# Performance work log

Measured on AMD Instinct MI355X. Metric: run time of the kernel, lower is better.

## Reference

```python
import jax, jax.numpy as jnp
import numpy as np

B, T, N, F_IN, F_OUT = 2, 8, 8192, 128, 32

def setup_inputs() -> dict:
    key = jax.random.key(0)
    k1, k2, k3, k4 = jax.random.split(key, 4)
    inp = jax.random.normal(k1, (B, T, N, F_IN), dtype=jnp.float32)
    adj = jax.random.randint(k2, (N, N), 0, 2, dtype=jnp.int32)
    # xavier_uniform with gain=1.414 ~ std = gain*sqrt(2/(fan_in+fan_out)); gaussian approx
    w_std = 1.414 * np.sqrt(2.0 / (F_IN + F_OUT))
    a_std = 1.414 * np.sqrt(2.0 / (2 * F_OUT + N))
    W = jax.random.normal(k3, (F_IN, F_OUT), dtype=jnp.float32) * w_std
    a = jax.random.normal(k4, (2 * F_OUT, N), dtype=jnp.float32) * a_std
    return {"inp": inp, "adj": adj, "W": W, "a": a}

def reference(inp, adj, W, a):
    # h: [B,T,N,out]
    h = jnp.einsum('btni,io->btno', inp, W)
    out = W.shape[1]
    # mask[j,i] = 1 if j is a neighbor of i (original: torch.where(adj[:, i] > 0))
    mask = (adj > 0).astype(h.dtype)
    # neighbor sum per destination node i: [B,T,N,out]
    nbr = jnp.einsum('ji,btjo->btio', mask, h)
    a1 = a[:out].T   # [N, out], per-node first half of attention vector
    a2 = a[out:].T   # [N, out], per-node second half
    # scalar score per (b,t,i); broadcast across j in the original attention matrix.
    # no-neighbor case coincides since nbr is zero there.
    s = jnp.einsum('btno,no->btn', h, a1) + jnp.einsum('btno,no->btn', nbr, a2)
    # h_prime[b,t,i,:] = s[b,t,i] * sum_j h[b,t,j,:]  (attention row is constant)
    h_prime = s[..., None] * jnp.sum(h, axis=2, keepdims=True)
    return jax.nn.relu(h_prime)
```

## Files before the change

### kernel.cpp

```cpp
#include <hip/hip_runtime.h>

#define BT 16
#define NN 8192
#define FIN 128
#define FOUT 32
#define NB 512
#define SPLITK 4
#define KSPAN (NN / SPLITK)
#define BKK 64
#define PADK 72

typedef __attribute__((ext_vector_type(8))) short short8;
typedef __attribute__((ext_vector_type(4))) float float4v;

__device__ __forceinline__ float bf2f(unsigned short u) {
    unsigned v = ((unsigned)u) << 16;
    float f;
    __builtin_memcpy(&f, &v, 4);
    return f;
}
__device__ __forceinline__ unsigned short f2bf(float f) {
    unsigned u;
    __builtin_memcpy(&u, &f, 4);
    u += 0x7FFFu + ((u >> 16) & 1u);
    return (unsigned short)(u >> 16);
}

__device__ __forceinline__ void load_lds16(const unsigned short* g, unsigned short* l) {
    __builtin_amdgcn_global_load_lds((const __attribute__((address_space(1))) void*)g,
                                     (__attribute__((address_space(3))) void*)l, 16, 0, 0);
}

__global__ void sniff_dtype(const unsigned* __restrict__ Wraw, unsigned* __restrict__ flag,
                            float* __restrict__ sumh) {
    int lane = threadIdx.x;
    unsigned u = Wraw[lane];
    float f = bf2f((unsigned short)(u & 0xFFFFu));
    float af = fabsf(f);
    bool plaus = (af > 1e-5f) && (af < 1e3f);
    unsigned long long msk = __ballot(plaus);
    if (lane == 0) flag[0] = (__popcll(msk) >= 32) ? 1u : 0u;
#pragma unroll
    for (int r = 0; r < 8; ++r) sumh[lane + 64 * r] = 0.f;
}

__launch_bounds__(256)
__global__ void k1(const void* __restrict__ inp_raw, const void* __restrict__ W_raw,
                   unsigned short* __restrict__ Ht, float* __restrict__ sumh,
                   float4* __restrict__ s2v, const unsigned* __restrict__ flagp) {
    __shared__ __align__(16) unsigned short Wt[32 * 136];
    int bid = blockIdx.x;
    const int tid = threadIdx.x;

    if (bid < 128) {
        float4 z; z.x = z.y = z.z = z.w = 0.f;
        s2v[bid * 256 + tid] = z;
        return;
    }
    bid -= 128;
    const int bt = bid >> 6;
    const int j0 = (bid & 63) * 128;
    const bool isbf = (*flagp != 0u);

    if (isbf) {
        const unsigned short* Wb = (const unsigned short*)W_raw;
#pragma unroll
        for (int r = 0; r < 16; ++r) {
            int idx = tid + 256 * r, i = idx >> 5, o = idx & 31;
            Wt[o * 136 + i] = Wb[idx];
        }
    } else {
        const float* Wf = (const float*)W_raw;
#pragma unroll
        for (int r = 0; r < 16; ++r) {
            int idx = tid + 256 * r, i = idx >> 5, o = idx & 31;
            Wt[o * 136 + i] = f2bf(Wf[idx]);
        }
    }
    __syncthreads();

    const int lane = tid & 63, w = tid >> 6;
    const int m = lane & 15, q = lane >> 4;
    const int mt = (w & 1) * 16;
    const int nt = (w >> 1) * 64;

    float4v acc[4];
#pragma unroll
    for (int c = 0; c < 4; ++c) { float4v z = {0.f, 0.f, 0.f, 0.f}; acc[c] = z; }

#pragma unroll
    for (int kstep = 0; kstep < 4; ++kstep) {
        short8 af = *(const short8*)&Wt[(mt + m) * 136 + kstep * 32 + q * 8];
#pragma unroll
        for (int c = 0; c < 4; ++c) {
            int j = j0 + nt + c * 16 + m;
            short8 bfrag;
            if (isbf) {
                bfrag = *(const short8*)((const unsigned short*)inp_raw +
                        ((size_t)bt * NN + j) * FIN + kstep * 32 + q * 8);
            } else {
                const float* fp = (const float*)inp_raw + ((size_t)bt * NN + j) * FIN + kstep * 32 + q * 8;
                float4 f0 = *(const float4*)fp;
                float4 f1 = *(const float4*)(fp + 4);
                union { unsigned short u[8]; short8 v; } t;
                t.u[0] = f2bf(f0.x); t.u[1] = f2bf(f0.y); t.u[2] = f2bf(f0.z); t.u[3] = f2bf(f0.w);
                t.u[4] = f2bf(f1.x); t.u[5] = f2bf(f1.y); t.u[6] = f2bf(f1.z); t.u[7] = f2bf(f1.w);
                bfrag = t.v;
            }
            acc[c] = __builtin_amdgcn_mfma_f32_16x16x32_bf16(af, bfrag, acc[c], 0, 0, 0);
        }
    }

#pragma unroll
    for (int c = 0; c < 4; ++c) {
#pragma unroll
        for (int e = 0; e < 4; ++e) {
            int o = mt + q * 4 + e;
            int j = j0 + nt + c * 16 + m;
            Ht[(size_t)(bt * FOUT + o) * NN + j] = f2bf(acc[c][e]);
        }
    }
#pragma unroll
    for (int e = 0; e < 4; ++e) {
        float s = acc[0][e] + acc[1][e] + acc[2][e] + acc[3][e];
        s += __shfl_xor(s, 1); s += __shfl_xor(s, 2);
        s += __shfl_xor(s, 4); s += __shfl_xor(s, 8);
        if (m == 0) atomicAdd(&sumh[bt * FOUT + mt + q * 4 + e], s);
    }
}

__launch_bounds__(512, 4)
__global__ void k2_fused(const int* __restrict__ adj, const unsigned short* __restrict__ Ht,
                         const void* __restrict__ a_raw, float* __restrict__ s2,
                         const unsigned* __restrict__ flagp) {
    __shared__ __align__(16) unsigned short As[64 * PADK];
    __shared__ __align__(16) unsigned short Bs[512 * 64];
    const int tid = threadIdx.x;
    const int lane = tid & 63;
    const int w = tid >> 6;
    const int m = lane & 15, q = lane >> 4;
    const int wn = w * 64;

    const int bid = blockIdx.x;
    const int xcd = bid & 7;
    const int z = xcd >> 1;
    const int ib = (bid >> 3) | ((xcd & 1) << 6);
    const int i0 = ib * 64;
    const int zbase = z * KSPAN;

    int boff[8];
#pragma unroll
    for (int c = 0; c < 8; ++c) {
        int u = (w * 8 + c) * 64 + lane;
        int n = u >> 3;
        int kbs = (u & 7) ^ (n & 7);
        boff[c] = n * NN + kbs * 8;
    }

    const int* gcol = adj + (zbase + w * 8) * NN + i0 + lane;

    float4v acc[4][4];
#pragma unroll
    for (int r = 0; r < 4; ++r)
#pragma unroll
        for (int c = 0; c < 4; ++c) { float4v zz = {0.f, 0.f, 0.f, 0.f}; acc[r][c] = zz; }

    int av[8];
#pragma unroll
    for (int kk = 0; kk < 8; ++kk)
        av[kk] = gcol[kk * NN];

    for (int ks0 = 0; ks0 < KSPAN; ks0 += BKK) {
        const int k0 = zbase + ks0;
        __builtin_amdgcn_s_barrier();
        __builtin_amdgcn_sched_barrier(0);
#pragma unroll
        for (int c = 0; c < 8; ++c)
            load_lds16(Ht + boff[c] + k0, &Bs[(w * 8 + c) * 512]);
        unsigned d0 = (av[0] > 0 ? 0x3F80u : 0u) | (av[1] > 0 ? 0x3F800000u : 0u);
        unsigned d1 = (av[2] > 0 ? 0x3F80u : 0u) | (av[3] > 0 ? 0x3F800000u : 0u);
        unsigned d2 = (av[4] > 0 ? 0x3F80u : 0u) | (av[5] > 0 ? 0x3F800000u : 0u);
        unsigned d3 = (av[6] > 0 ? 0x3F80u : 0u) | (av[7] > 0 ? 0x3F800000u : 0u);
        const int ksn = (ks0 + BKK < KSPAN) ? ks0 + BKK : 0;
#pragma unroll
        for (int kk = 0; kk < 8; ++kk)
            av[kk] = gcol[(ksn + kk) * NN];
        {
            int4 t;
            t.x = (int)d0; t.y = (int)d1; t.z = (int)d2; t.w = (int)d3;
            *(int4*)&As[lane * PADK + w * 8] = t;
        }
        asm volatile("s_waitcnt vmcnt(8) lgkmcnt(0)" ::: "memory");
        __builtin_amdgcn_sched_barrier(0);
        __builtin_amdgcn_s_barrier();
        __builtin_amdgcn_sched_barrier(0);
#pragma unroll
        for (int ks = 0; ks < 2; ++ks) {
            short8 af[4];
#pragma unroll
            for (int r = 0; r < 4; ++r)
                af[r] = *(const short8*)&As[(r * 16 + m) * PADK + ks * 32 + q * 8];
#pragma unroll
            for (int c = 0; c < 4; ++c) {
                int row = wn + c * 16 + m;
                int kbs = (ks * 4 + q) ^ (m & 7);
                short8 bfr = *(const short8*)&Bs[row * 64 + kbs * 8];
#pragma unroll
                for (int r = 0; r < 4; ++r)
                    acc[r][c] = __builtin_amdgcn_mfma_f32_16x16x32_bf16(af[r], bfr, acc[r][c], 0, 0, 0);
            }
        }
    }
    asm volatile("" :: "v"(av[0]), "v"(av[1]), "v"(av[2]), "v"(av[3]),
                       "v"(av[4]), "v"(av[5]), "v"(av[6]), "v"(av[7]));

    const bool isbf = (*flagp != 0u);
    const int btA = wn >> 5;
#pragma unroll
    for (int r = 0; r < 4; ++r) {
#pragma unroll
        for (int e = 0; e < 4; ++e) {
            int gi = i0 + r * 16 + q * 4 + e;
            float a2m, a2m16;
            if (isbf) {
                const unsigned short* ab = (const unsigned short*)a_raw;
                a2m   = bf2f(ab[(size_t)(FOUT + m) * NN + gi]);
                a2m16 = bf2f(ab[(size_t)(FOUT + 16 + m) * NN + gi]);
            } else {
                const float* afp = (const float*)a_raw;
                a2m   = afp[(size_t)(FOUT + m) * NN + gi];
                a2m16 = afp[(size_t)(FOUT + 16 + m) * NN + gi];
            }
            float sA = acc[r][0][e] * a2m + acc[r][1][e] * a2m16;
            float sB = acc[r][2][e] * a2m + acc[r][3][e] * a2m16;
            sA += __shfl_xor(sA, 1); sA += __shfl_xor(sA, 2);
            sA += __shfl_xor(sA, 4); sA += __shfl_xor(sA, 8);
            sB += __shfl_xor(sB, 1); sB += __shfl_xor(sB, 2);
            sB += __shfl_xor(sB, 4); sB += __shfl_xor(sB, 8);
            if (m == 0) {
                atomicAdd(&s2[(size_t)btA * NN + gi], sA);
                atomicAdd(&s2[(size_t)(btA + 1) * NN + gi], sB);
            }
        }
    }
}

__launch_bounds__(256)
__global__ void k3_out(const unsigned short* __restrict__ Ht, const float* __restrict__ s2,
                       const float* __restrict__ sumh, const void* __restrict__ a_raw,
                       void* __restrict__ out_raw, const unsigned* __restrict__ flagp) {
    const int i = blockIdx.x * 256 + threadIdx.x;
    const int bt = blockIdx.y;
    const bool isbf = (*flagp != 0u);

    float s = s2[(size_t)bt * NN + i];
    if (isbf) {
        const unsigned short* ab = (const unsigned short*)a_raw;
#pragma unroll
        for (int o = 0; o < 32; ++o) {
            float h = bf2f(Ht[(size_t)(bt * FOUT + o) * NN + i]);
            s += h * bf2f(ab[(size_t)o * NN + i]);
        }
    } else {
        const float* afp = (const float*)a_raw;
#pragma unroll
        for (int o = 0; o < 32; ++o) {
            float h = bf2f(Ht[(size_t)(bt * FOUT + o) * NN + i]);
            s += h * afp[(size_t)o * NN + i];
        }
    }

    float ov[32];
#pragma unroll
    for (int o = 0; o < 32; ++o) ov[o] = fmaxf(s * sumh[bt * FOUT + o], 0.f);

    size_t ob = ((size_t)bt * NN + i) * FOUT;
    if (isbf) {
        unsigned short* o16 = (unsigned short*)out_raw + ob;
#pragma unroll
        for (int c = 0; c < 8; ++c) {
            ushort4 p;
            p.x = f2bf(ov[c * 4 + 0]); p.y = f2bf(ov[c * 4 + 1]);
            p.z = f2bf(ov[c * 4 + 2]); p.w = f2bf(ov[c * 4 + 3]);
            *(ushort4*)(o16 + c * 4) = p;
        }
    } else {
        float* of = (float*)out_raw + ob;
#pragma unroll
        for (int c = 0; c < 8; ++c) {
            float4 v;
            v.x = ov[c * 4 + 0]; v.y = ov[c * 4 + 1]; v.z = ov[c * 4 + 2]; v.w = ov[c * 4 + 3];
            *(float4*)(of + c * 4) = v;
        }
    }
}

extern "C" void kernel_launch(void* const* d_in, const int* in_sizes, int n_in,
                              void* d_out, int out_size, void* d_ws, size_t ws_size,
                              hipStream_t stream) {
    const void* inp = d_in[0];
    const int* adj = (const int*)d_in[1];
    const void* W = d_in[2];
    const void* a = d_in[3];

    char* ws = (char*)d_ws;
    unsigned short* Ht = (unsigned short*)ws;
    unsigned* flag = (unsigned*)(ws + 8388608);
    float* s2 = (float*)(ws + 8388608 + 4096);
    float* sumh = (float*)(ws + 8388608 + 4096 + 524288);

    sniff_dtype<<<1, 64, 0, stream>>>((const unsigned*)W, flag, sumh);
    k1<<<1152, 256, 0, stream>>>(inp, W, Ht, sumh, (float4*)s2, flag);
    k2_fused<<<512, 512, 0, stream>>>(adj, Ht, a, s2, flag);
    k3_out<<<dim3(NN / 256, BT), 256, 0, stream>>>(Ht, s2, sumh, a, d_out, flag);
}
```

Measured before the change: 482.7 us.

## Fuse output epilogue into split-K GEMM via last-block ticket counter

Removes the separate k3_out launch. Each of the split-K blocks for a row tile takes a ticket with an atomic, and the last one to finish reads the reduced s2, adds the h·a1 term and writes the ReLU output for its 64 nodes. The change also moves sched_barriers so the mask computation can overlap the LDS loads. This saves one launch and a pass over s2, at the cost of a serialized tail in 128 blocks plus extra threadfences.

```diff
diff --git a/kernel.cpp b/kernel.cpp
--- a/kernel.cpp
+++ b/kernel.cpp
@@ -32,7 +32,7 @@
 }
 
 __global__ void sniff_dtype(const unsigned* __restrict__ Wraw, unsigned* __restrict__ flag,
-                            float* __restrict__ sumh) {
+                            float* __restrict__ sumh, int* __restrict__ ticket) {
     int lane = threadIdx.x;
     unsigned u = Wraw[lane];
     float f = bf2f((unsigned short)(u & 0xFFFFu));
@@ -42,6 +42,8 @@
     if (lane == 0) flag[0] = (__popcll(msk) >= 32) ? 1u : 0u;
 #pragma unroll
     for (int r = 0; r < 8; ++r) sumh[lane + 64 * r] = 0.f;
+    ticket[lane] = 0;
+    ticket[lane + 64] = 0;
 }
 
 __launch_bounds__(256)
@@ -132,9 +134,11 @@
 __launch_bounds__(512, 4)
 __global__ void k2_fused(const int* __restrict__ adj, const unsigned short* __restrict__ Ht,
                          const void* __restrict__ a_raw, float* __restrict__ s2,
-                         const unsigned* __restrict__ flagp) {
+                         const float* __restrict__ sumh, int* __restrict__ ticket,
+                         void* __restrict__ out_raw, const unsigned* __restrict__ flagp) {
     __shared__ __align__(16) unsigned short As[64 * PADK];
     __shared__ __align__(16) unsigned short Bs[512 * 64];
+    __shared__ int s_last;
     const int tid = threadIdx.x;
     const int lane = tid & 63;
     const int w = tid >> 6;
@@ -177,6 +181,7 @@
 #pragma unroll
         for (int c = 0; c < 8; ++c)
             load_lds16(Ht + boff[c] + k0, &Bs[(w * 8 + c) * 512]);
+        __builtin_amdgcn_sched_barrier(0);
         unsigned d0 = (av[0] > 0 ? 0x3F80u : 0u) | (av[1] > 0 ? 0x3F800000u : 0u);
         unsigned d1 = (av[2] > 0 ? 0x3F80u : 0u) | (av[3] > 0 ? 0x3F800000u : 0u);
         unsigned d2 = (av[4] > 0 ? 0x3F80u : 0u) | (av[5] > 0 ? 0x3F800000u : 0u);
@@ -191,9 +196,7 @@
             *(int4*)&As[lane * PADK + w * 8] = t;
         }
         asm volatile("s_waitcnt vmcnt(8) lgkmcnt(0)" ::: "memory");
-        __builtin_amdgcn_sched_barrier(0);
         __builtin_amdgcn_s_barrier();
-        __builtin_amdgcn_sched_barrier(0);
 #pragma unroll
         for (int ks = 0; ks < 2; ++ks) {
             short8 af[4];
@@ -243,54 +246,55 @@
             }
         }
     }
-}
-
-__launch_bounds__(256)
-__global__ void k3_out(const unsigned short* __restrict__ Ht, const float* __restrict__ s2,
-                       const float* __restrict__ sumh, const void* __restrict__ a_raw,
-                       void* __restrict__ out_raw, const unsigned* __restrict__ flagp) {
-    const int i = blockIdx.x * 256 + threadIdx.x;
-    const int bt = blockIdx.y;
-    const bool isbf = (*flagp != 0u);
-
-    float s = s2[(size_t)bt * NN + i];
-    if (isbf) {
-        const unsigned short* ab = (const unsigned short*)a_raw;
-#pragma unroll
-        for (int o = 0; o < 32; ++o) {
-            float h = bf2f(Ht[(size_t)(bt * FOUT + o) * NN + i]);
-            s += h * bf2f(ab[(size_t)o * NN + i]);
-        }
-    } else {
-        const float* afp = (const float*)a_raw;
-#pragma unroll
-        for (int o = 0; o < 32; ++o) {
-            float h = bf2f(Ht[(size_t)(bt * FOUT + o) * NN + i]);
-            s += h * afp[(size_t)o * NN + i];
-        }
-    }
-
-    float ov[32];
-#pragma unroll
-    for (int o = 0; o < 32; ++o) ov[o] = fmaxf(s * sumh[bt * FOUT + o], 0.f);
-
-    size_t ob = ((size_t)bt * NN + i) * FOUT;
-    if (isbf) {
-        unsigned short* o16 = (unsigned short*)out_raw + ob;
-#pragma unroll
-        for (int c = 0; c < 8; ++c) {
-            ushort4 p;
-            p.x = f2bf(ov[c * 4 + 0]); p.y = f2bf(ov[c * 4 + 1]);
-            p.z = f2bf(ov[c * 4 + 2]); p.w = f2bf(ov[c * 4 + 3]);
-            *(ushort4*)(o16 + c * 4) = p;
-        }
-    } else {
-        float* of = (float*)out_raw + ob;
-#pragma unroll
-        for (int c = 0; c < 8; ++c) {
-            float4 v;
-            v.x = ov[c * 4 + 0]; v.y = ov[c * 4 + 1]; v.z = ov[c * 4 + 2]; v.w = ov[c * 4 + 3];
-            *(float4*)(of + c * 4) = v;
+
+    __threadfence();
+    __syncthreads();
+    if (tid == 0) s_last = (atomicAdd(&ticket[ib], 1) == SPLITK - 1) ? 1 : 0;
+    __syncthreads();
+    if (!s_last) return;
+    __threadfence();
+
+    for (int p = tid; p < BT * 64; p += 512) {
+        const int bt = p >> 6;
+        const int i = i0 + (p & 63);
+        float st = __hip_atomic_load(&s2[(size_t)bt * NN + i],
+                                     __ATOMIC_RELAXED, __HIP_MEMORY_SCOPE_AGENT);
+        float h1 = 0.f;
+        if (isbf) {
+            const unsigned short* ab = (const unsigned short*)a_raw;
+#pragma unroll
+            for (int o = 0; o < 32; ++o)
+                h1 += bf2f(Ht[(size_t)(bt * FOUT + o) * NN + i]) * bf2f(ab[(size_t)o * NN + i]);
+        } else {
+            const float* afp = (const float*)a_raw;
+#pragma unroll
+            for (int o = 0; o < 32; ++o)
+                h1 += bf2f(Ht[(size_t)(bt * FOUT + o) * NN + i]) * afp[(size_t)o * NN + i];
+        }
+        st += h1;
+        size_t ob = ((size_t)bt * NN + i) * FOUT;
+        if (isbf) {
+            unsigned short* o16 = (unsigned short*)out_raw + ob;
+#pragma unroll
+            for (int c = 0; c < 8; ++c) {
+                ushort4 pk;
+                pk.x = f2bf(fmaxf(st * sumh[bt * FOUT + c * 4 + 0], 0.f));
+                pk.y = f2bf(fmaxf(st * sumh[bt * FOUT + c * 4 + 1], 0.f));
+                pk.z = f2bf(fmaxf(st * sumh[bt * FOUT + c * 4 + 2], 0.f));
+                pk.w = f2bf(fmaxf(st * sumh[bt * FOUT + c * 4 + 3], 0.f));
+                *(ushort4*)(o16 + c * 4) = pk;
+            }
+        } else {
+            float* of = (float*)out_raw + ob;
+#pragma unroll
+            for (int c = 0; c < 8; ++c) {
+                float4 v;
+                v.x = fmaxf(st * sumh[bt * FOUT + c * 4 + 0], 0.f);
+                v.y = fmaxf(st * sumh[bt * FOUT + c * 4 + 1], 0.f);
+                v.z = fmaxf(st * sumh[bt * FOUT + c * 4 + 2], 0.f);
+                v.w = fmaxf(st * sumh[bt * FOUT + c * 4 + 3], 0.f);
+                *(float4*)(of + c * 4) = v;
+            }
         }
     }
 }
@@ -308,9 +312,9 @@
     unsigned* flag = (unsigned*)(ws + 8388608);
     float* s2 = (float*)(ws + 8388608 + 4096);
     float* sumh = (float*)(ws + 8388608 + 4096 + 524288);
-
-    sniff_dtype<<<1, 64, 0, stream>>>((const unsigned*)W, flag, sumh);
+    int* ticket = (int*)(ws + 8388608 + 4096 + 524288 + 2048);
+
+    sniff_dtype<<<1, 64, 0, stream>>>((const unsigned*)W, flag, sumh, ticket);
     k1<<<1152, 256, 0, stream>>>(inp, W, Ht, sumh, (float4*)s2, flag);
-    k2_fused<<<512, 512, 0, stream>>>(adj, Ht, a, s2, flag);
-    k3_out<<<dim3(NN / 256, BT), 256, 0, stream>>>(Ht, s2, sumh, a, d_out, flag);
-}
+    k2_fused<<<512, 512, 0, stream>>>(adj, Ht, a, s2, sumh, ticket, d_out, flag);
+}
```

Result: slower. 701.6 us (+45.3%).
